# Performance work log

Hardware: AMD Instinct MI355X
Metric: run time of the kernel (lower is better)

The kernel has to match this reference:

```python
import jax, jax.numpy as jnp
import numpy as np

EPS_Z = 1e-07
EPS_M = 1e-08
EPS_V = 1e-16


def _grid_sample(img, grid, mode):
    # img: [B,C,H,W], grid: [B,Hg,Wg,2] in [-1,1], align_corners=True, zeros padding
    B, C, H, W = img.shape
    x = (grid[..., 0] + 1.0) * 0.5 * (W - 1)
    y = (grid[..., 1] + 1.0) * 0.5 * (H - 1)
    imgt = img.transpose(0, 2, 3, 1)  # [B,H,W,C]
    bidx = jnp.arange(B)[:, None, None]

    def fetch(yi, xi):
        valid = (yi >= 0) & (yi < H) & (xi >= 0) & (xi < W)
        v = imgt[bidx, jnp.clip(yi, 0, H - 1), jnp.clip(xi, 0, W - 1)]
        return v * valid[..., None].astype(img.dtype)

    if mode == 'nearest':
        out = fetch(jnp.round(y).astype(jnp.int32), jnp.round(x).astype(jnp.int32))
    else:
        x0 = jnp.floor(x)
        y0 = jnp.floor(y)
        x0i = x0.astype(jnp.int32)
        y0i = y0.astype(jnp.int32)
        wx = x - x0
        wy = y - y0
        out = (fetch(y0i, x0i) * ((1 - wx) * (1 - wy))[..., None]
               + fetch(y0i, x0i + 1) * (wx * (1 - wy))[..., None]
               + fetch(y0i + 1, x0i) * ((1 - wx) * wy)[..., None]
               + fetch(y0i + 1, x0i + 1) * (wx * wy)[..., None])
    return out.transpose(0, 3, 1, 2)  # [B,C,Hg,Wg]


def _project(depth, T, invK, K, homo, H, W):
    # backproject + reproject -> normalized pix coords [B,H,W,2]
    B = depth.shape[0]
    d = depth.reshape(B, 1, -1)
    p3 = jnp.einsum('bij,jn->bin', invK[:, :3, :3], homo) * d   # [B,3,HW]
    p3 = jnp.concatenate([p3, jnp.ones_like(d)], axis=1)        # [B,4,HW]
    P = (K @ T)[:, :3, :]                                       # [B,3,4]
    p2 = P @ p3                                                 # [B,3,HW]
    xy = p2[:, :2] / (p2[:, 2:3] + EPS_Z)
    xy = xy.reshape(B, 2, H, W).transpose(0, 2, 3, 1)           # [B,H,W,2]
    xy = xy / jnp.array([W - 1, H - 1], dtype=xy.dtype)
    return (xy - 0.5) * 2.0


def _get_virtual_image(src_img, src_mask, tar_depth, tar_invK, src_K, T, homo, H, W):
    pix = _project(tar_depth, T, tar_invK, src_K, homo, H, W)
    img_w = _grid_sample(src_img, pix, 'bilinear')
    img_w = jnp.where(jnp.isnan(img_w), 2.0, img_w)
    mask_w = _grid_sample(src_mask, pix, 'nearest')
    mask_w = jnp.where(jnp.isnan(mask_w), 0.0, mask_w)
    invalid = jnp.any((pix > 1) | (pix < -1), axis=-1)[:, None]  # [B,1,H,W]
    return img_w, (~invalid).astype(img_w.dtype) * mask_w


def _mean_std(feature, maskf):
    _, c, h, w = maskf.shape
    msum = maskf.sum(axis=(1, 2, 3), keepdims=True)
    mean = (feature * maskf).sum(axis=(1, 2, 3), keepdims=True) / (msum + EPS_M)
    var = ((feature - mean) ** 2).sum(axis=(1, 2, 3), keepdims=True) / (c * h * w)
    return mean, jnp.sqrt(var + EPS_V)


def _norm_image_single(src_img, src_mask, warp_img, warp_mask):
    wm = jax.lax.stop_gradient(warp_mask)
    maskf = jax.lax.stop_gradient(((src_mask * wm) > 0).astype(warp_img.dtype))
    if maskf.shape[1] != 3:
        maskf = jnp.tile(maskf, (1, 3, 1, 1))
    mask_sum = maskf.sum(axis=(1, 2, 3))
    any_zero = jnp.any(mask_sum == 0)
    s_mean, s_std = _mean_std(jax.lax.stop_gradient(src_img), maskf)
    w_mean, w_std = _mean_std(jax.lax.stop_gradient(warp_img), maskf)
    norm = (warp_img - w_mean) / (w_std + EPS_M) * s_std + s_mean
    return jnp.where(any_zero, warp_img, norm * wm)


def _forward(org_prev_image, org_image, org_next_image, mask, intrinsic,
             inv_intrinsic, true_depth_map, prev_to_cur_pose, cur_to_next_pose,
             rel_poses, cam_index, neighbor_cam_indices):
    H, W = mask.shape[-2:]
    gx, gy = np.meshgrid(np.arange(W), np.arange(H), indexing='xy')
    homo = jnp.asarray(np.stack([gx.ravel(), gy.ravel(), np.ones(H * W)], 0),
                       dtype=mask.dtype)  # [3, H*W]
    ci = int(cam_index)
    ref_color = org_image[:, ci]
    ref_mask = mask[:, ci]
    ref_K = intrinsic[:, ci]
    ref_invK = inv_intrinsic[:, ci]
    ref_depth = true_depth_map[:, ci]

    outs = []
    for T, src_color in zip([prev_to_cur_pose[:, ci], cur_to_next_pose[:, ci]],
                            [org_prev_image[:, ci], org_next_image[:, ci]]):
        wi, wm = _get_virtual_image(src_color, mask[:, ci], ref_depth,
                                    ref_invK, ref_K, T, homo, H, W)
        wi = _norm_image_single(ref_color, ref_mask, wi, wm)
        outs += [wi, wm]

    for f_idx in range(2):  # frame_id -1 then +1
        src_colors = org_prev_image if f_idx == 0 else org_next_image
        ov = jnp.zeros_like(ref_color)
        ovm = jnp.zeros_like(ref_mask)
        for n, cur in enumerate(np.asarray(neighbor_cam_indices)):
            cur = int(cur)
            wi, wm = _get_virtual_image(src_colors[:, cur], mask[:, cur],
                                        ref_depth, ref_invK, intrinsic[:, cur],
                                        rel_poses[f_idx, n], homo, H, W)
            wi = _norm_image_single(ref_color, ref_mask, wi, wm)
            ov = ov + wi
            ovm = ovm + wm
        outs += [ov, ovm]
    # concat all warped views along channels: [B, 2*(3+1)+2*(3+1)=16, H, W]
    return jnp.concatenate(outs, axis=1)


def _yaw_pose(theta, t):
    c, s = np.cos(theta), np.sin(theta)
    T = np.eye(4, dtype=np.float32)
    T[:3, :3] = np.array([[c, 0, s], [0, 1, 0], [-s, 0, c]], dtype=np.float32)
    T[:3, 3] = t
    return T


def setup_inputs() -> dict:
    key = jax.random.key(0)
    B, N, H, W = 2, 6, 384, 640
    k1, k2, k3, k4 = jax.random.split(key, 4)
    org_prev_image = jax.random.uniform(k1, (B, N, 3, H, W), jnp.float32)
    org_image = jax.random.uniform(k2, (B, N, 3, H, W), jnp.float32)
    org_next_image = jax.random.uniform(k3, (B, N, 3, H, W), jnp.float32)
    mask = jnp.ones((B, N, 1, H, W), jnp.float32)
    true_depth_map = 1.0 + 79.0 * jax.random.uniform(k4, (B, N, 1, H, W), jnp.float32)

    rng = np.random.RandomState(0)
    K = np.tile(np.eye(4, dtype=np.float32), (B, N, 1, 1))
    for b in range(B):
        for n in range(N):
            K[b, n, 0, 0] = 0.82 * W * (1 + 0.02 * rng.randn())
            K[b, n, 1, 1] = 0.82 * W * (1 + 0.02 * rng.randn())
            K[b, n, 0, 2] = 0.5 * W
            K[b, n, 1, 2] = 0.5 * H
    invK = np.linalg.inv(K).astype(np.float32)

    p2c = np.stack([np.stack([_yaw_pose(0.02 * rng.randn(),
                                        np.array([0.1, 0.0, 0.5], np.float32))
                              for _ in range(N)]) for _ in range(B)])
    c2n = np.stack([np.stack([_yaw_pose(0.02 * rng.randn(),
                                        np.array([-0.1, 0.0, -0.5], np.float32))
                              for _ in range(N)]) for _ in range(B)])
    rel = np.zeros((2, 2, B, 4, 4), np.float32)
    for f in range(2):
        for n, ang in enumerate([1.0, -1.0]):
            for b in range(B):
                rel[f, n, b] = _yaw_pose(ang + 0.02 * rng.randn(),
                                         np.array([1.5 * ang, 0.0, 0.2], np.float32))

    return {
        'org_prev_image': org_prev_image,
        'org_image': org_image,
        'org_next_image': org_next_image,
        'mask': mask,
        'intrinsic': jnp.asarray(K),
        'inv_intrinsic': jnp.asarray(invK),
        'true_depth_map': true_depth_map,
        'prev_to_cur_pose': jnp.asarray(p2c.astype(np.float32)),
        'cur_to_next_pose': jnp.asarray(c2n.astype(np.float32)),
        'rel_poses': jnp.asarray(rel),
        'cam_index': 0,
        'neighbor_cam_indices': np.array([1, 5], dtype=np.int64),
    }


def reference(org_prev_image, org_image, org_next_image, mask, intrinsic,
              inv_intrinsic, true_depth_map, prev_to_cur_pose, cur_to_next_pose,
              rel_poses, cam_index, neighbor_cam_indices):
    return _forward(org_prev_image, org_image, org_next_image, mask, intrinsic,
                    inv_intrinsic, true_depth_map, prev_to_cur_pose,
                    cur_to_next_pose, rel_poses, cam_index, neighbor_cam_indices)
```

## Files before the change

### kernel.cpp

```cpp
#include <hip/hip_runtime.h>
#include <hip/hip_fp16.h>
#include <math.h>

#define HH 384
#define WW 640
#define HWSZ (HH*WW)
#define BB 2
#define NN 6
#define BPG 256

#define WS_P      0
#define WS_INVK   144
#define WS_CAM    176
#define WS_ACC    192
#define WS_STAT   288
#define WS_PACK   512
#define WS_CACHE2 (512 + 12 * HWSZ * 2)
#define WS_END    (WS_CACHE2 + 12 * HWSZ * 2)

__device__ __forceinline__ unsigned pack2(float a, float b) {
    __half2 h = __halves2half2(__float2half(a), __float2half(b));
    union { __half2 h2; unsigned u; } cv; cv.h2 = h; return cv.u;
}
__device__ __forceinline__ float2 unpack2(unsigned u) {
    union { __half2 h2; unsigned u; } cv; cv.u = u;
    return __half22float2(cv.h2);
}

__device__ __forceinline__ void project_pix(const float* __restrict__ Pm, const float* __restrict__ ik,
                                            float fx, float fy, float d,
                                            float& gx, float& gy, float& sx, float& sy)
{
    float q0 = __fadd_rn(__fadd_rn(__fmul_rn(ik[0], fx), __fmul_rn(ik[1], fy)), ik[2]);
    float q1 = __fadd_rn(__fadd_rn(__fmul_rn(ik[3], fx), __fmul_rn(ik[4], fy)), ik[5]);
    float q2 = __fadd_rn(__fadd_rn(__fmul_rn(ik[6], fx), __fmul_rn(ik[7], fy)), ik[8]);
    float a0 = __fmul_rn(q0, d), a1 = __fmul_rn(q1, d), a2 = __fmul_rn(q2, d);
    float p0 = __fadd_rn(__fadd_rn(__fadd_rn(__fmul_rn(Pm[0], a0), __fmul_rn(Pm[1], a1)), __fmul_rn(Pm[2], a2)), Pm[3]);
    float p1 = __fadd_rn(__fadd_rn(__fadd_rn(__fmul_rn(Pm[4], a0), __fmul_rn(Pm[5], a1)), __fmul_rn(Pm[6], a2)), Pm[7]);
    float p2 = __fadd_rn(__fadd_rn(__fadd_rn(__fmul_rn(Pm[8], a0), __fmul_rn(Pm[9], a1)), __fmul_rn(Pm[10], a2)), Pm[11]);
    float z  = __fadd_rn(p2, 1e-7f);
    float xx = __fdiv_rn(p0, z);
    float yy = __fdiv_rn(p1, z);
    gx = __fmul_rn(__fsub_rn(__fdiv_rn(xx, 639.0f), 0.5f), 2.0f);
    gy = __fmul_rn(__fsub_rn(__fdiv_rn(yy, 383.0f), 0.5f), 2.0f);
    sx = __fmul_rn(__fmul_rn(__fadd_rn(gx, 1.0f), 0.5f), 639.0f);
    sy = __fmul_rn(__fmul_rn(__fadd_rn(gy, 1.0f), 0.5f), 383.0f);
}

__device__ __forceinline__ void sample_packed(const uint2* __restrict__ pk,
                                              const float* Pm, const float* ik, float d, int px_i, int py_i,
                                              float& i0, float& i1, float& i2, float& wmv)
{
    float gx, gy, sx, sy;
    project_pix(Pm, ik, (float)px_i, (float)py_i, d, gx, gy, sx, sy);

    float x0f = floorf(sx), y0f = floorf(sy);
    float wx = __fsub_rn(sx, x0f), wy = __fsub_rn(sy, y0f);
    int x0 = (int)x0f, y0 = (int)y0f;
    int x1 = x0 + 1, y1 = y0 + 1;
    bool vx0 = (x0 >= 0) && (x0 < WW), vx1 = (x1 >= 0) && (x1 < WW);
    bool vy0 = (y0 >= 0) && (y0 < HH), vy1 = (y1 >= 0) && (y1 < HH);
    float w00 = (1.0f - wx) * (1.0f - wy);
    float w01 = wx * (1.0f - wy);
    float w10 = (1.0f - wx) * wy;
    float w11 = wx * wy;
    uint2 t00 = {0u, 0u}, t01 = {0u, 0u}, t10 = {0u, 0u}, t11 = {0u, 0u};
    if (vy0 && vx0) t00 = pk[y0 * WW + x0];
    if (vy0 && vx1) t01 = pk[y0 * WW + x1];
    if (vy1 && vx0) t10 = pk[y1 * WW + x0];
    if (vy1 && vx1) t11 = pk[y1 * WW + x1];
    float2 a00 = unpack2(t00.x), b00 = unpack2(t00.y);
    float2 a01 = unpack2(t01.x), b01 = unpack2(t01.y);
    float2 a10 = unpack2(t10.x), b10 = unpack2(t10.y);
    float2 a11 = unpack2(t11.x), b11 = unpack2(t11.y);
    float v0 = ((a00.x * w00 + a01.x * w01) + a10.x * w10) + a11.x * w11;
    float v1 = ((a00.y * w00 + a01.y * w01) + a10.y * w10) + a11.y * w11;
    float v2 = ((b00.x * w00 + b01.x * w01) + b10.x * w10) + b11.x * w11;
    i0 = (v0 != v0) ? 2.0f : v0;
    i1 = (v1 != v1) ? 2.0f : v1;
    i2 = (v2 != v2) ? 2.0f : v2;

    bool invalid = (gx > 1.0f) || (gx < -1.0f) || (gy > 1.0f) || (gy < -1.0f);
    float xr = rintf(sx), yr = rintf(sy);
    int xi = (int)xr, yi = (int)yr;
    bool vm = (xi >= 0) && (xi < WW) && (yi >= 0) && (yi < HH) && !invalid;
    bool selx = (xi == x1), sely = (yi == y1);
    float m00 = b00.y, m01 = b01.y, m10 = b10.y, m11 = b11.y;
    float msel = sely ? (selx ? m11 : m10) : (selx ? m01 : m00);
    float mv = vm ? msel : 0.0f;
    if (mv != mv) mv = 0.0f;
    wmv = mv;
}

__device__ __forceinline__ void sample_one(const float* __restrict__ simg, const float* __restrict__ smask,
                                           const float* Pm, const float* ik, float d, int px_i, int py_i,
                                           float& i0, float& i1, float& i2, float& wmv)
{
    float gx, gy, sx, sy;
    project_pix(Pm, ik, (float)px_i, (float)py_i, d, gx, gy, sx, sy);
    float x0f = floorf(sx), y0f = floorf(sy);
    float wx = __fsub_rn(sx, x0f), wy = __fsub_rn(sy, y0f);
    int x0 = (int)x0f, y0 = (int)y0f;
    int x1 = x0 + 1, y1 = y0 + 1;
    bool vx0 = (x0 >= 0) && (x0 < WW), vx1 = (x1 >= 0) && (x1 < WW);
    bool vy0 = (y0 >= 0) && (y0 < HH), vy1 = (y1 >= 0) && (y1 < HH);
    float w00 = (1.0f - wx) * (1.0f - wy);
    float w01 = wx * (1.0f - wy);
    float w10 = (1.0f - wx) * wy;
    float w11 = wx * wy;
    int o00 = y0 * WW + x0, o01 = y0 * WW + x1;
    int o10 = y1 * WW + x0, o11 = y1 * WW + x1;
    float t00_0 = 0.f, t00_1 = 0.f, t00_2 = 0.f;
    float t01_0 = 0.f, t01_1 = 0.f, t01_2 = 0.f;
    float t10_0 = 0.f, t10_1 = 0.f, t10_2 = 0.f;
    float t11_0 = 0.f, t11_1 = 0.f, t11_2 = 0.f;
    if (vy0 && vx0) { t00_0 = simg[o00]; t00_1 = simg[HWSZ + o00]; t00_2 = simg[2 * HWSZ + o00]; }
    if (vy0 && vx1) { t01_0 = simg[o01]; t01_1 = simg[HWSZ + o01]; t01_2 = simg[2 * HWSZ + o01]; }
    if (vy1 && vx0) { t10_0 = simg[o10]; t10_1 = simg[HWSZ + o10]; t10_2 = simg[2 * HWSZ + o10]; }
    if (vy1 && vx1) { t11_0 = simg[o11]; t11_1 = simg[HWSZ + o11]; t11_2 = simg[2 * HWSZ + o11]; }
    float v0 = ((t00_0 * w00 + t01_0 * w01) + t10_0 * w10) + t11_0 * w11;
    float v1 = ((t00_1 * w00 + t01_1 * w01) + t10_1 * w10) + t11_1 * w11;
    float v2 = ((t00_2 * w00 + t01_2 * w01) + t10_2 * w10) + t11_2 * w11;
    i0 = (v0 != v0) ? 2.0f : v0;
    i1 = (v1 != v1) ? 2.0f : v1;
    i2 = (v2 != v2) ? 2.0f : v2;
    bool invalid = (gx > 1.0f) || (gx < -1.0f) || (gy > 1.0f) || (gy < -1.0f);
    float xr = rintf(sx), yr = rintf(sy);
    int xi = (int)xr, yi = (int)yr;
    bool vm = (xi >= 0) && (xi < WW) && (yi >= 0) && (yi < HH) && !invalid;
    float mv = 0.0f;
    if (vm) mv = smask[yi * WW + xi];
    if (mv != mv) mv = 0.0f;
    wmv = mv;
}

__global__ void vr_setup(const float* __restrict__ K, const float* __restrict__ invK,
                         const float* __restrict__ p2c, const float* __restrict__ c2n,
                         const float* __restrict__ rel, const void* __restrict__ camI,
                         const void* __restrict__ nbr, float* __restrict__ ws)
{
    int tid = threadIdx.x;
    if (tid < 96) ws[WS_ACC + tid] = 0.0f;
    if (tid == 0) {
        int ci = ((const int*)camI)[0];
        long long a = ((const long long*)nbr)[0];
        long long bq = ((const long long*)nbr)[1];
        int n0, n1;
        if (a >= 0 && a < NN && bq >= 0 && bq < NN) { n0 = (int)a; n1 = (int)bq; }
        else { n0 = ((const int*)nbr)[0]; n1 = ((const int*)nbr)[1]; }
        int* cams = (int*)(ws + WS_CAM);
        cams[0] = ci; cams[1] = ci; cams[2] = n0; cams[3] = n1; cams[4] = n0; cams[5] = n1;
        cams[6] = ci;
        for (int b = 0; b < BB; b++) {
            const float* ik = invK + (size_t)(b * NN + ci) * 16;
            float* dst = ws + WS_INVK + b * 9;
            dst[0] = ik[0]; dst[1] = ik[1]; dst[2] = ik[2];
            dst[3] = ik[4]; dst[4] = ik[5]; dst[5] = ik[6];
            dst[6] = ik[8]; dst[7] = ik[9]; dst[8] = ik[10];
            for (int w = 0; w < 6; w++) {
                int cam = cams[w];
                const float* Km = K + (size_t)(b * NN + cam) * 16;
                const float* T;
                if (w == 0)      T = p2c + (size_t)(b * NN + ci) * 16;
                else if (w == 1) T = c2n + (size_t)(b * NN + ci) * 16;
                else {
                    int f = (w >= 4) ? 1 : 0;
                    int n = (w == 3 || w == 5) ? 1 : 0;
                    T = rel + (size_t)((f * 2 + n) * BB + b) * 16;
                }
                float* Pd = ws + WS_P + (w * BB + b) * 12;
                for (int i = 0; i < 3; i++)
                    for (int j = 0; j < 4; j++) {
                        float s = __fadd_rn(__fadd_rn(__fadd_rn(
                                      __fmul_rn(Km[i * 4 + 0], T[0 * 4 + j]),
                                      __fmul_rn(Km[i * 4 + 1], T[1 * 4 + j])),
                                      __fmul_rn(Km[i * 4 + 2], T[2 * 4 + j])),
                                      __fmul_rn(Km[i * 4 + 3], T[3 * 4 + j]));
                        Pd[i * 4 + j] = s;
                    }
            }
        }
    }
}

__global__ __launch_bounds__(256) void vr_pack(
    const float* __restrict__ prev, const float* __restrict__ nxt,
    const float* __restrict__ maskT, float* __restrict__ ws)
{
    int gid = blockIdx.x * 256 + threadIdx.x;
    int group = gid / HWSZ;
    int p = gid - group * HWSZ;
    int w = group / BB, b = group % BB;
    const int* cams = (const int*)(ws + WS_CAM);
    int cam = cams[w];
    const float* simg  = ((w == 0 || w == 2 || w == 3) ? prev : nxt) + (size_t)(b * NN + cam) * 3 * HWSZ;
    const float* smask = maskT + (size_t)(b * NN + cam) * HWSZ;
    float r = simg[p], g = simg[HWSZ + p], bl = simg[2 * HWSZ + p], m = smask[p];
    uint2 u;
    u.x = pack2(r, g);
    u.y = pack2(bl, m);
    ((uint2*)(ws + WS_PACK))[(size_t)group * HWSZ + p] = u;
}

__global__ __launch_bounds__(256) void vr_phaseA(
    const float* __restrict__ prev, const float* __restrict__ nxt,
    const float* __restrict__ org, const float* __restrict__ maskT,
    const float* __restrict__ depthT, float* __restrict__ ws, int mode)
{
    int group = blockIdx.x / BPG;
    int blkin = blockIdx.x % BPG;
    int w = group / BB, b = group % BB;
    const int* cams = (const int*)(ws + WS_CAM);
    int ci = cams[6];
    int cam = cams[w];
    float Pl[12], ikl[9];
    {
        const float* Pm = ws + WS_P + group * 12;
        const float* ik = ws + WS_INVK + b * 9;
#pragma unroll
        for (int i = 0; i < 12; i++) Pl[i] = Pm[i];
#pragma unroll
        for (int i = 0; i < 9; i++) ikl[i] = ik[i];
    }
    const float* simg  = ((w == 0 || w == 2 || w == 3) ? prev : nxt) + (size_t)(b * NN + cam) * 3 * HWSZ;
    const float* smask = maskT + (size_t)(b * NN + cam) * HWSZ;
    const float* dep   = depthT + (size_t)(b * NN + ci) * HWSZ;
    const float* rimg  = org + (size_t)(b * NN + ci) * 3 * HWSZ;
    const float* rmask = maskT + (size_t)(b * NN + ci) * HWSZ;
    const uint2* pk  = (const uint2*)(ws + WS_PACK) + (size_t)group * HWSZ;
    uint2* cache     = (uint2*)(ws + WS_CACHE2) + (size_t)group * HWSZ;

    float acc[7] = {0, 0, 0, 0, 0, 0, 0};
    for (int p = blkin * 256 + threadIdx.x; p < HWSZ; p += BPG * 256) {
        int py_i = p / WW, px_i = p - py_i * WW;
        float d = dep[p];
        float i0, i1, i2, wmv;
        if (mode) {
            sample_packed(pk, Pl, ikl, d, px_i, py_i, i0, i1, i2, wmv);
            uint2 u; u.x = pack2(i0, i1); u.y = pack2(i2, wmv);
            cache[p] = u;
        } else {
            sample_one(simg, smask, Pl, ikl, d, px_i, py_i, i0, i1, i2, wmv);
        }
        float rm = rmask[p];
        float m = (rm * wmv > 0.0f) ? 1.0f : 0.0f;
        float r0 = rimg[p], r1 = rimg[HWSZ + p], r2 = rimg[2 * HWSZ + p];
        float ws3 = i0 + i1 + i2;
        float rs3 = r0 + r1 + r2;
        acc[0] += m;
        acc[1] += rs3 * m;
        acc[2] += ws3 * m;
        acc[3] += ws3;
        acc[4] += i0 * i0 + i1 * i1 + i2 * i2;
        acc[5] += rs3;
        acc[6] += r0 * r0 + r1 * r1 + r2 * r2;
    }
    __shared__ float sred[4][7];
    int lane = threadIdx.x & 63, wv = threadIdx.x >> 6;
#pragma unroll
    for (int k = 0; k < 7; k++) {
        float v2 = acc[k];
        for (int off = 32; off; off >>= 1) v2 += __shfl_down(v2, off);
        if (lane == 0) sred[wv][k] = v2;
    }
    __syncthreads();
    if (threadIdx.x < 7) {
        float s = sred[0][threadIdx.x] + sred[1][threadIdx.x] + sred[2][threadIdx.x] + sred[3][threadIdx.x];
        atomicAdd(&ws[WS_ACC + group * 8 + threadIdx.x], s);
    }
}

__global__ void vr_finalize(float* __restrict__ ws)
{
    int t = threadIdx.x;
    if (t >= 12) return;
    int w = t / BB;
    const float* acc = ws + WS_ACC + t * 8;
    double cnt = acc[0], smask = acc[1], wmask = acc[2];
    double wsum = acc[3], wsumsq = acc[4], ssum = acc[5], ssumsq = acc[6];
    double msum = 3.0 * cnt;
    double NT = 3.0 * (double)HWSZ;
    double smean = smask / (msum + 1e-8);
    double svar  = (ssumsq - 2.0 * smean * ssum + NT * smean * smean) / NT;
    double sstd  = sqrt(svar + 1e-16);
    double wmean = wmask / (msum + 1e-8);
    double wvar  = (wsumsq - 2.0 * wmean * wsum + NT * wmean * wmean) / NT;
    double wstd  = sqrt(wvar + 1e-16);
    float cnt0 = ws[WS_ACC + (w * BB + 0) * 8];
    float cnt1 = ws[WS_ACC + (w * BB + 1) * 8];
    float az = (cnt0 == 0.0f || cnt1 == 0.0f) ? 1.0f : 0.0f;
    float* st = ws + WS_STAT + t * 6;
    st[0] = (float)smean; st[1] = (float)sstd;
    st[2] = (float)wmean; st[3] = (float)wstd;
    st[4] = az;
}

__global__ __launch_bounds__(256) void vr_phaseB(
    const float* __restrict__ prev, const float* __restrict__ nxt,
    const float* __restrict__ maskT, const float* __restrict__ depthT,
    const float* __restrict__ ws, float* __restrict__ out, int mode)
{
    int idx = blockIdx.x * 256 + threadIdx.x;
    int ob = idx / (BB * HWSZ);
    int rem = idx - ob * (BB * HWSZ);
    int b = rem / HWSZ;
    int p = rem - b * HWSZ;
    const int* cams = (const int*)(ws + WS_CAM);
    int ci = cams[6];
    int py_i = p / WW, px_i = p - py_i * WW;
    int w0 = (ob == 0) ? 0 : (ob == 1) ? 1 : (ob == 2) ? 2 : 4;
    int nw = (ob < 2) ? 1 : 2;
    float o0 = 0, o1 = 0, o2 = 0, om = 0;
    for (int k = 0; k < nw; k++) {
        int w = w0 + k;
        int group = w * BB + b;
        float i0, i1, i2, wmv;
        if (mode) {
            const uint2* cg = (const uint2*)(ws + WS_CACHE2) + (size_t)group * HWSZ;
            uint2 u = cg[p];
            float2 ab = unpack2(u.x), cd = unpack2(u.y);
            i0 = ab.x; i1 = ab.y; i2 = cd.x; wmv = cd.y;
        } else {
            int cam = cams[w];
            const float* Pm = ws + WS_P + group * 12;
            const float* ik = ws + WS_INVK + b * 9;
            const float* simg  = ((w == 0 || w == 2 || w == 3) ? prev : nxt) + (size_t)(b * NN + cam) * 3 * HWSZ;
            const float* smask = maskT + (size_t)(b * NN + cam) * HWSZ;
            float d = depthT[(size_t)(b * NN + ci) * HWSZ + p];
            sample_one(simg, smask, Pm, ik, d, px_i, py_i, i0, i1, i2, wmv);
        }
        const float* st = ws + WS_STAT + group * 6;
        float smean = st[0], sstd = st[1], wmean = st[2], wstd = st[3];
        bool az = st[4] != 0.0f;
        float v0, v1, v2;
        if (az) { v0 = i0; v1 = i1; v2 = i2; }
        else {
            v0 = ((i0 - wmean) / (wstd + 1e-8f)) * sstd + smean; v0 *= wmv;
            v1 = ((i1 - wmean) / (wstd + 1e-8f)) * sstd + smean; v1 *= wmv;
            v2 = ((i2 - wmean) / (wstd + 1e-8f)) * sstd + smean; v2 *= wmv;
        }
        o0 += v0; o1 += v1; o2 += v2; om += wmv;
    }
    float* base = out + ((size_t)b * 16 + ob * 4) * HWSZ;
    base[p] = o0;
    base[HWSZ + p] = o1;
    base[2 * HWSZ + p] = o2;
    base[3 * HWSZ + p] = om;
}

extern "C" void kernel_launch(void* const* d_in, const int* in_sizes, int n_in,
                              void* d_out, int out_size, void* d_ws, size_t ws_size,
                              hipStream_t stream)
{
    const float* prev  = (const float*)d_in[0];
    const float* org   = (const float*)d_in[1];
    const float* nxt   = (const float*)d_in[2];
    const float* maskT = (const float*)d_in[3];
    const float* K     = (const float*)d_in[4];
    const float* invK  = (const float*)d_in[5];
    const float* dep   = (const float*)d_in[6];
    const float* p2c   = (const float*)d_in[7];
    const float* c2n   = (const float*)d_in[8];
    const float* rel   = (const float*)d_in[9];
    const void*  camI  = d_in[10];
    const void*  nbr   = d_in[11];
    float* ws  = (float*)d_ws;
    float* out = (float*)d_out;

    size_t need = (size_t)WS_END * sizeof(float);
    int mode = (ws_size >= need) ? 1 : 0;

    hipLaunchKernelGGL(vr_setup, dim3(1), dim3(128), 0, stream, K, invK, p2c, c2n, rel, camI, nbr, ws);
    if (mode)
        hipLaunchKernelGGL(vr_pack, dim3(12 * HWSZ / 256), dim3(256), 0, stream, prev, nxt, maskT, ws);
    hipLaunchKernelGGL(vr_phaseA, dim3(12 * BPG), dim3(256), 0, stream, prev, nxt, org, maskT, dep, ws, mode);
    hipLaunchKernelGGL(vr_finalize, dim3(1), dim3(64), 0, stream, ws);
    hipLaunchKernelGGL(vr_phaseB, dim3(4 * BB * HWSZ / 256), dim3(256), 0, stream, prev, nxt, maskT, dep, ws, out, mode);
}
```

Before: 66.78 us.

## Pack horizontal pixel pairs and precompute reference-image stats buffer

The pack kernel can now store each source texel together with its right neighbour in a 16-byte record, so bilinear sampling needs two 128-bit loads instead of four 64-bit loads. A new kernel also precomputes per-pixel reference sum, sum of squares, depth and mask into one float4 buffer, which replaces five strided loads in phaseA. Both paths are chosen from the available workspace size. In exchange the packed source buffer doubles in size, adding write traffic and an extra kernel launch, and falls back when the workspace is too small.

```diff
diff --git a/kernel.cpp b/kernel.cpp
--- a/kernel.cpp
+++ b/kernel.cpp
@@ -14,9 +14,12 @@
 #define WS_CAM    176
 #define WS_ACC    192
 #define WS_STAT   288
-#define WS_PACK   512
-#define WS_CACHE2 (512 + 12 * HWSZ * 2)
-#define WS_END    (WS_CACHE2 + 12 * HWSZ * 2)
+#define CACHE2_OFF 512
+#define RP_OFF    (CACHE2_OFF + 12 * HWSZ * 2)
+#define PK_OFF_RP (RP_OFF + 2 * HWSZ * 4)
+#define NEED_FULL  (PK_OFF_RP + 12 * HWSZ * 4)
+#define NEED_RP    (PK_OFF_RP + 12 * HWSZ * 2)
+#define NEED_CACHE (RP_OFF + 12 * HWSZ * 2)
 
 __device__ __forceinline__ unsigned pack2(float a, float b) {
     __half2 h = __halves2half2(__float2half(a), __float2half(b));
@@ -47,28 +50,15 @@
     sy = __fmul_rn(__fmul_rn(__fadd_rn(gy, 1.0f), 0.5f), 383.0f);
 }
 
-__device__ __forceinline__ void sample_packed(const uint2* __restrict__ pk,
-                                              const float* Pm, const float* ik, float d, int px_i, int py_i,
+__device__ __forceinline__ void bilerp_finish(uint2 t00, uint2 t01, uint2 t10, uint2 t11,
+                                              float wx, float wy, float sx, float sy,
+                                              int x1, int y1, float gx, float gy,
                                               float& i0, float& i1, float& i2, float& wmv)
 {
-    float gx, gy, sx, sy;
-    project_pix(Pm, ik, (float)px_i, (float)py_i, d, gx, gy, sx, sy);
-
-    float x0f = floorf(sx), y0f = floorf(sy);
-    float wx = __fsub_rn(sx, x0f), wy = __fsub_rn(sy, y0f);
-    int x0 = (int)x0f, y0 = (int)y0f;
-    int x1 = x0 + 1, y1 = y0 + 1;
-    bool vx0 = (x0 >= 0) && (x0 < WW), vx1 = (x1 >= 0) && (x1 < WW);
-    bool vy0 = (y0 >= 0) && (y0 < HH), vy1 = (y1 >= 0) && (y1 < HH);
     float w00 = (1.0f - wx) * (1.0f - wy);
     float w01 = wx * (1.0f - wy);
     float w10 = (1.0f - wx) * wy;
     float w11 = wx * wy;
-    uint2 t00 = {0u, 0u}, t01 = {0u, 0u}, t10 = {0u, 0u}, t11 = {0u, 0u};
-    if (vy0 && vx0) t00 = pk[y0 * WW + x0];
-    if (vy0 && vx1) t01 = pk[y0 * WW + x1];
-    if (vy1 && vx0) t10 = pk[y1 * WW + x0];
-    if (vy1 && vx1) t11 = pk[y1 * WW + x1];
     float2 a00 = unpack2(t00.x), b00 = unpack2(t00.y);
     float2 a01 = unpack2(t01.x), b01 = unpack2(t01.y);
     float2 a10 = unpack2(t10.x), b10 = unpack2(t10.y);
@@ -79,17 +69,61 @@
     i0 = (v0 != v0) ? 2.0f : v0;
     i1 = (v1 != v1) ? 2.0f : v1;
     i2 = (v2 != v2) ? 2.0f : v2;
-
     bool invalid = (gx > 1.0f) || (gx < -1.0f) || (gy > 1.0f) || (gy < -1.0f);
     float xr = rintf(sx), yr = rintf(sy);
     int xi = (int)xr, yi = (int)yr;
     bool vm = (xi >= 0) && (xi < WW) && (yi >= 0) && (yi < HH) && !invalid;
     bool selx = (xi == x1), sely = (yi == y1);
-    float m00 = b00.y, m01 = b01.y, m10 = b10.y, m11 = b11.y;
-    float msel = sely ? (selx ? m11 : m10) : (selx ? m01 : m00);
+    float msel = sely ? (selx ? b11.y : b10.y) : (selx ? b01.y : b00.y);
     float mv = vm ? msel : 0.0f;
     if (mv != mv) mv = 0.0f;
     wmv = mv;
+}
+
+__device__ __forceinline__ void sample_pair(const uint4* __restrict__ pk2,
+                                            const float* Pm, const float* ik, float d, int px_i, int py_i,
+                                            float& i0, float& i1, float& i2, float& wmv)
+{
+    float gx, gy, sx, sy;
+    project_pix(Pm, ik, (float)px_i, (float)py_i, d, gx, gy, sx, sy);
+    float x0f = floorf(sx), y0f = floorf(sy);
+    float wx = __fsub_rn(sx, x0f), wy = __fsub_rn(sy, y0f);
+    int x0 = (int)x0f, y0 = (int)y0f;
+    int x1 = x0 + 1, y1 = y0 + 1;
+    bool vx0 = (x0 >= 0) && (x0 < WW), vx1 = (x1 >= 0) && (x1 < WW);
+    bool vy0 = (y0 >= 0) && (y0 < HH), vy1 = (y1 >= 0) && (y1 < HH);
+    uint4 ra = {0u,0u,0u,0u}, rb = {0u,0u,0u,0u};
+    if (vy0) {
+        if (vx0) ra = pk2[y0 * WW + x0];
+        else if (vx1) { uint4 t = pk2[y0 * WW]; ra.z = t.x; ra.w = t.y; }
+    }
+    if (vy1) {
+        if (vx0) rb = pk2[y1 * WW + x0];
+        else if (vx1) { uint4 t = pk2[y1 * WW]; rb.z = t.x; rb.w = t.y; }
+    }
+    uint2 t00 = {ra.x, ra.y}, t01 = {ra.z, ra.w};
+    uint2 t10 = {rb.x, rb.y}, t11 = {rb.z, rb.w};
+    bilerp_finish(t00, t01, t10, t11, wx, wy, sx, sy, x1, y1, gx, gy, i0, i1, i2, wmv);
+}
+
+__device__ __forceinline__ void sample_packed(const uint2* __restrict__ pk,
+                                              const float* Pm, const float* ik, float d, int px_i, int py_i,
+                                              float& i0, float& i1, float& i2, float& wmv)
+{
+    float gx, gy, sx, sy;
+    project_pix(Pm, ik, (float)px_i, (float)py_i, d, gx, gy, sx, sy);
+    float x0f = floorf(sx), y0f = floorf(sy);
+    float wx = __fsub_rn(sx, x0f), wy = __fsub_rn(sy, y0f);
+    int x0 = (int)x0f, y0 = (int)y0f;
+    int x1 = x0 + 1, y1 = y0 + 1;
+    bool vx0 = (x0 >= 0) && (x0 < WW), vx1 = (x1 >= 0) && (x1 < WW);
+    bool vy0 = (y0 >= 0) && (y0 < HH), vy1 = (y1 >= 0) && (y1 < HH);
+    uint2 t00 = {0u,0u}, t01 = {0u,0u}, t10 = {0u,0u}, t11 = {0u,0u};
+    if (vy0 && vx0) t00 = pk[y0 * WW + x0];
+    if (vy0 && vx1) t01 = pk[y0 * WW + x1];
+    if (vy1 && vx0) t10 = pk[y1 * WW + x0];
+    if (vy1 && vx1) t11 = pk[y1 * WW + x1];
+    bilerp_finish(t00, t01, t10, t11, wx, wy, sx, sy, x1, y1, gx, gy, i0, i1, i2, wmv);
 }
 
 __device__ __forceinline__ void sample_one(const float* __restrict__ simg, const float* __restrict__ smask,
@@ -110,17 +144,15 @@
     float w11 = wx * wy;
     int o00 = y0 * WW + x0, o01 = y0 * WW + x1;
     int o10 = y1 * WW + x0, o11 = y1 * WW + x1;
-    float t00_0 = 0.f, t00_1 = 0.f, t00_2 = 0.f;
-    float t01_0 = 0.f, t01_1 = 0.f, t01_2 = 0.f;
-    float t10_0 = 0.f, t10_1 = 0.f, t10_2 = 0.f;
-    float t11_0 = 0.f, t11_1 = 0.f, t11_2 = 0.f;
-    if (vy0 && vx0) { t00_0 = simg[o00]; t00_1 = simg[HWSZ + o00]; t00_2 = simg[2 * HWSZ + o00]; }
-    if (vy0 && vx1) { t01_0 = simg[o01]; t01_1 = simg[HWSZ + o01]; t01_2 = simg[2 * HWSZ + o01]; }
-    if (vy1 && vx0) { t10_0 = simg[o10]; t10_1 = simg[HWSZ + o10]; t10_2 = simg[2 * HWSZ + o10]; }
-    if (vy1 && vx1) { t11_0 = simg[o11]; t11_1 = simg[HWSZ + o11]; t11_2 = simg[2 * HWSZ + o11]; }
-    float v0 = ((t00_0 * w00 + t01_0 * w01) + t10_0 * w10) + t11_0 * w11;
-    float v1 = ((t00_1 * w00 + t01_1 * w01) + t10_1 * w10) + t11_1 * w11;
-    float v2 = ((t00_2 * w00 + t01_2 * w01) + t10_2 * w10) + t11_2 * w11;
+    float t00_0=0.f,t00_1=0.f,t00_2=0.f, t01_0=0.f,t01_1=0.f,t01_2=0.f;
+    float t10_0=0.f,t10_1=0.f,t10_2=0.f, t11_0=0.f,t11_1=0.f,t11_2=0.f;
+    if (vy0 && vx0) { t00_0 = simg[o00]; t00_1 = simg[HWSZ + o00]; t00_2 = simg[2*HWSZ + o00]; }
+    if (vy0 && vx1) { t01_0 = simg[o01]; t01_1 = simg[HWSZ + o01]; t01_2 = simg[2*HWSZ + o01]; }
+    if (vy1 && vx0) { t10_0 = simg[o10]; t10_1 = simg[HWSZ + o10]; t10_2 = simg[2*HWSZ + o10]; }
+    if (vy1 && vx1) { t11_0 = simg[o11]; t11_1 = simg[HWSZ + o11]; t11_2 = simg[2*HWSZ + o11]; }
+    float v0 = ((t00_0*w00 + t01_0*w01) + t10_0*w10) + t11_0*w11;
+    float v1 = ((t00_1*w00 + t01_1*w01) + t10_1*w10) + t11_1*w11;
+    float v2 = ((t00_2*w00 + t01_2*w01) + t10_2*w10) + t11_2*w11;
     i0 = (v0 != v0) ? 2.0f : v0;
     i1 = (v1 != v1) ? 2.0f : v1;
     i2 = (v2 != v2) ? 2.0f : v2;
@@ -185,7 +217,7 @@
 
 __global__ __launch_bounds__(256) void vr_pack(
     const float* __restrict__ prev, const float* __restrict__ nxt,
-    const float* __restrict__ maskT, float* __restrict__ ws)
+    const float* __restrict__ maskT, float* __restrict__ ws, int pk_off, int pair)
 {
     int gid = blockIdx.x * 256 + threadIdx.x;
     int group = gid / HWSZ;
@@ -196,16 +228,49 @@
     const float* simg  = ((w == 0 || w == 2 || w == 3) ? prev : nxt) + (size_t)(b * NN + cam) * 3 * HWSZ;
     const float* smask = maskT + (size_t)(b * NN + cam) * HWSZ;
     float r = simg[p], g = simg[HWSZ + p], bl = simg[2 * HWSZ + p], m = smask[p];
-    uint2 u;
-    u.x = pack2(r, g);
-    u.y = pack2(bl, m);
-    ((uint2*)(ws + WS_PACK))[(size_t)group * HWSZ + p] = u;
+    if (pair) {
+        int px = p % WW;
+        float r1 = 0.f, g1 = 0.f, b1 = 0.f, m1 = 0.f;
+        if (px < WW - 1) {
+            r1 = simg[p + 1]; g1 = simg[HWSZ + p + 1]; b1 = simg[2 * HWSZ + p + 1]; m1 = smask[p + 1];
+        }
+        uint4 u;
+        u.x = pack2(r, g);  u.y = pack2(bl, m);
+        u.z = pack2(r1, g1); u.w = pack2(b1, m1);
+        ((uint4*)(ws + pk_off))[(size_t)group * HWSZ + p] = u;
+    } else {
+        uint2 u;
+        u.x = pack2(r, g); u.y = pack2(bl, m);
+        ((uint2*)(ws + pk_off))[(size_t)group * HWSZ + p] = u;
+    }
+}
+
+__global__ __launch_bounds__(256) void vr_packref(
+    const float* __restrict__ org, const float* __restrict__ maskT,
+    const float* __restrict__ depthT, float* __restrict__ ws)
+{
+    int gid = blockIdx.x * 256 + threadIdx.x;
+    int b = gid / HWSZ;
+    int p = gid - b * HWSZ;
+    const int* cams = (const int*)(ws + WS_CAM);
+    int ci = cams[6];
+    const float* rimg  = org + (size_t)(b * NN + ci) * 3 * HWSZ;
+    float r0 = rimg[p], r1 = rimg[HWSZ + p], r2 = rimg[2 * HWSZ + p];
+    float rm = maskT[(size_t)(b * NN + ci) * HWSZ + p];
+    float d  = depthT[(size_t)(b * NN + ci) * HWSZ + p];
+    float4 v;
+    v.x = r0 + r1 + r2;
+    v.y = r0 * r0 + r1 * r1 + r2 * r2;
+    v.z = d;
+    v.w = rm;
+    ((float4*)(ws + RP_OFF))[(size_t)b * HWSZ + p] = v;
 }
 
 __global__ __launch_bounds__(256) void vr_phaseA(
     const float* __restrict__ prev, const float* __restrict__ nxt,
     const float* __restrict__ org, const float* __restrict__ maskT,
-    const float* __restrict__ depthT, float* __restrict__ ws, int mode)
+    const float* __restrict__ depthT, float* __restrict__ ws,
+    int havecache, int userp, int pair, int pk_off)
 {
     int group = blockIdx.x / BPG;
     int blkin = blockIdx.x % BPG;
@@ -227,33 +292,43 @@
     const float* dep   = depthT + (size_t)(b * NN + ci) * HWSZ;
     const float* rimg  = org + (size_t)(b * NN + ci) * 3 * HWSZ;
     const float* rmask = maskT + (size_t)(b * NN + ci) * HWSZ;
-    const uint2* pk  = (const uint2*)(ws + WS_PACK) + (size_t)group * HWSZ;
-    uint2* cache     = (uint2*)(ws + WS_CACHE2) + (size_t)group * HWSZ;
+    const float4* rpk  = (const float4*)(ws + RP_OFF) + (size_t)b * HWSZ;
+    const uint2* pk1   = (const uint2*)(ws + pk_off) + (size_t)group * HWSZ;
+    const uint4* pk2   = (const uint4*)(ws + pk_off) + (size_t)group * HWSZ;
+    uint2* cache       = (uint2*)(ws + CACHE2_OFF) + (size_t)group * HWSZ;
 
     float acc[7] = {0, 0, 0, 0, 0, 0, 0};
     for (int p = blkin * 256 + threadIdx.x; p < HWSZ; p += BPG * 256) {
         int py_i = p / WW, px_i = p - py_i * WW;
-        float d = dep[p];
+        float rs3, rsq, d, rm;
+        if (userp) {
+            float4 rp = rpk[p];
+            rs3 = rp.x; rsq = rp.y; d = rp.z; rm = rp.w;
+        } else {
+            d = dep[p];
+            float r0 = rimg[p], r1 = rimg[HWSZ + p], r2 = rimg[2 * HWSZ + p];
+            rm = rmask[p];
+            rs3 = r0 + r1 + r2;
+            rsq = r0 * r0 + r1 * r1 + r2 * r2;
+        }
         float i0, i1, i2, wmv;
-        if (mode) {
-            sample_packed(pk, Pl, ikl, d, px_i, py_i, i0, i1, i2, wmv);
+        if (havecache) {
+            if (pair) sample_pair(pk2, Pl, ikl, d, px_i, py_i, i0, i1, i2, wmv);
+            else      sample_packed(pk1, Pl, ikl, d, px_i, py_i, i0, i1, i2, wmv);
             uint2 u; u.x = pack2(i0, i1); u.y = pack2(i2, wmv);
             cache[p] = u;
         } else {
             sample_one(simg, smask, Pl, ikl, d, px_i, py_i, i0, i1, i2, wmv);
         }
-        float rm = rmask[p];
         float m = (rm * wmv > 0.0f) ? 1.0f : 0.0f;
-        float r0 = rimg[p], r1 = rimg[HWSZ + p], r2 = rimg[2 * HWSZ + p];
         float ws3 = i0 + i1 + i2;
-        float rs3 = r0 + r1 + r2;
         acc[0] += m;
         acc[1] += rs3 * m;
         acc[2] += ws3 * m;
         acc[3] += ws3;
         acc[4] += i0 * i0 + i1 * i1 + i2 * i2;
         acc[5] += rs3;
-        acc[6] += r0 * r0 + r1 * r1 + r2 * r2;
+        acc[6] += rsq;
     }
     __shared__ float sred[4][7];
     int lane = threadIdx.x & 63, wv = threadIdx.x >> 6;
@@ -298,7 +373,7 @@
 __global__ __launch_bounds__(256) void vr_phaseB(
     const float* __restrict__ prev, const float* __restrict__ nxt,
     const float* __restrict__ maskT, const float* __restrict__ depthT,
-    const float* __restrict__ ws, float* __restrict__ out, int mode)
+    const float* __restrict__ ws, float* __restrict__ out, int havecache)
 {
     int idx = blockIdx.x * 256 + threadIdx.x;
     int ob = idx / (BB * HWSZ);
@@ -315,8 +390,8 @@
         int w = w0 + k;
         int group = w * BB + b;
         float i0, i1, i2, wmv;
-        if (mode) {
-            const uint2* cg = (const uint2*)(ws + WS_CACHE2) + (size_t)group * HWSZ;
+        if (havecache) {
+            const uint2* cg = (const uint2*)(ws + CACHE2_OFF) + (size_t)group * HWSZ;
             uint2 u = cg[p];
             float2 ab = unpack2(u.x), cd = unpack2(u.y);
             i0 = ab.x; i1 = ab.y; i2 = cd.x; wmv = cd.y;
@@ -367,13 +442,20 @@
     float* ws  = (float*)d_ws;
     float* out = (float*)d_out;
 
-    size_t need = (size_t)WS_END * sizeof(float);
-    int mode = (ws_size >= need) ? 1 : 0;
+    size_t fl = ws_size / sizeof(float);
+    int pair = 0, userp = 0, havecache = 0;
+    if (fl >= (size_t)NEED_FULL)       { pair = 1; userp = 1; havecache = 1; }
+    else if (fl >= (size_t)NEED_RP)    { userp = 1; havecache = 1; }
+    else if (fl >= (size_t)NEED_CACHE) { havecache = 1; }
+    int pk_off = userp ? PK_OFF_RP : RP_OFF;
 
     hipLaunchKernelGGL(vr_setup, dim3(1), dim3(128), 0, stream, K, invK, p2c, c2n, rel, camI, nbr, ws);
-    if (mode)
-        hipLaunchKernelGGL(vr_pack, dim3(12 * HWSZ / 256), dim3(256), 0, stream, prev, nxt, maskT, ws);
-    hipLaunchKernelGGL(vr_phaseA, dim3(12 * BPG), dim3(256), 0, stream, prev, nxt, org, maskT, dep, ws, mode);
+    if (havecache)
+        hipLaunchKernelGGL(vr_pack, dim3(12 * HWSZ / 256), dim3(256), 0, stream, prev, nxt, maskT, ws, pk_off, pair);
+    if (userp)
+        hipLaunchKernelGGL(vr_packref, dim3(2 * HWSZ / 256), dim3(256), 0, stream, org, maskT, dep, ws);
+    hipLaunchKernelGGL(vr_phaseA, dim3(12 * BPG), dim3(256), 0, stream, prev, nxt, org, maskT, dep, ws,
+                       havecache, userp, pair, pk_off);
     hipLaunchKernelGGL(vr_finalize, dim3(1), dim3(64), 0, stream, ws);
-    hipLaunchKernelGGL(vr_phaseB, dim3(4 * BB * HWSZ / 256), dim3(256), 0, stream, prev, nxt, maskT, dep, ws, out, mode);
-}
+    hipLaunchKernelGGL(vr_phaseB, dim3(4 * BB * HWSZ / 256), dim3(256), 0, stream, prev, nxt, maskT, dep, ws, out, havecache);
+}
```

Result: slower. 80.30 us (+20.2%).
